# Kernel tuning notes

Hardware: AMD Instinct MI355X
Metric: run time of the kernel (lower is better)

## Reference

```python
import jax, jax.numpy as jnp
import numpy as np

BSZ, H, P, L = 8, 512, 128, 8192
DT_MIN, DT_MAX = 1e-3, 1e-1


def setup_inputs() -> dict:
    key = jax.random.key(0)
    ks = jax.random.split(key, 6)
    inp = {}
    inp["input_sequence"] = jax.random.normal(ks[0], (BSZ, 1, H, 1, L), jnp.float32)
    # HiPPO-like init: negative real parts, pi*k imaginary parts
    inp["Lambda_re"] = -jax.random.uniform(ks[1], (P,), jnp.float32, 0.1, 1.0)
    inp["Lambda_im"] = jnp.pi * jnp.arange(P, dtype=jnp.float32)
    # lecun_normal-ish: fan_in = H for B, fan_in = P for C (real+imag parts)
    inp["B"] = jax.random.normal(ks[2], (P, H, 2), jnp.float32) / np.float32(np.sqrt(2 * H))
    inp["C"] = jax.random.normal(ks[3], (H, P, 2), jnp.float32) / np.float32(np.sqrt(2 * P))
    inp["D"] = jax.random.normal(ks[4], (H,), jnp.float32)
    u01 = jax.random.uniform(ks[5], (P, 1), jnp.float32)
    inp["log_step"] = u01 * np.float32(np.log(DT_MAX) - np.log(DT_MIN)) + np.float32(np.log(DT_MIN))
    return inp


def _binary_operator(q_i, q_j):
    A_i, b_i = q_i
    A_j, b_j = q_j
    return (A_j * A_i, A_j * b_i + b_j)


def reference(input_sequence, Lambda_re, Lambda_im, B, C, D, log_step):
    # (bsz, 1, H, 1, L) -> (bsz, L, H)
    u = input_sequence[:, 0, :, 0].transpose(0, 2, 1)

    Lambda = Lambda_re + 1j * Lambda_im                      # (P,)
    B_tilde = B[..., 0] + 1j * B[..., 1]                     # (P, H)
    C_tilde = C[..., 0] + 1j * C[..., 1]                     # (H, P)
    step = jnp.exp(log_step[:, 0])                           # (P,)

    # zero-order hold discretization
    Lambda_bar = jnp.exp(Lambda * step)                      # (P,)
    B_bar = ((Lambda_bar - 1.0) / Lambda)[:, None] * B_tilde # (P, H)

    Bu = jnp.einsum('blh,ph->blp', u, B_bar)                 # (bsz, L, P) complex
    Lambda_elems = jnp.broadcast_to(Lambda_bar, Bu.shape)
    _, xs = jax.lax.associative_scan(_binary_operator, (Lambda_elems, Bu), axis=1)

    # conj_sym=True -> factor of 2 on the real part of emissions
    ys = 2.0 * jnp.einsum('blp,hp->blh', xs, C_tilde).real + D * u
    ys = jax.nn.gelu(ys, approximate=False)

    # back to (bsz, 1, H, 1, L)
    return ys.transpose(0, 2, 1)[:, None, :, None, :]
```

## Files before the change

### kernel.cpp

```cpp
#include <hip/hip_runtime.h>
#include <hip/hip_bf16.h>
#include <cmath>

namespace {
constexpr int Pn = 128;
constexpr int Hn = 512;
constexpr int Ln = 8192;
constexpr int BS = 8;
constexpr size_t OFF_BMAT = 2048;
constexpr size_t OFF_CMAT = 264192;
constexpr size_t OFF_PPOW = 526336;
constexpr size_t OFF_END  = 591872;
constexpr size_t OFF_CAR  = 1640448;
constexpr size_t HEADB    = 2689024;
constexpr size_t SZ_BU = (size_t)256 * Ln * 2;
}

typedef __attribute__((ext_vector_type(4))) float f32x4;
typedef __attribute__((ext_vector_type(8))) short bf16x8;

static __device__ inline short f2bf(float x) {
  __hip_bfloat16 h = __float2bfloat16(x);
  return *(short*)&h;
}
static __device__ inline float bf2f(short s) {
  unsigned u = ((unsigned)(unsigned short)s) << 16;
  return __uint_as_float(u);
}

static __device__ inline void async_copy16(const void* g, void* l) {
  __builtin_amdgcn_global_load_lds(
      (const __attribute__((address_space(1))) unsigned int*)g,
      (__attribute__((address_space(3))) unsigned int*)l, 16, 0, 0);
}

__global__ void precompute_kernel(const float* __restrict__ Lre,
                                  const float* __restrict__ Lim,
                                  const float* __restrict__ Bin,
                                  const float* __restrict__ Cin,
                                  const float* __restrict__ lstep,
                                  float* __restrict__ Lam,
                                  __hip_bfloat16* __restrict__ Bmat,
                                  __hip_bfloat16* __restrict__ Cmat,
                                  float* __restrict__ Ppow) {
  int tid = blockIdx.x * blockDim.x + threadIdx.x;
  if (tid < 2 * Pn * Hn) {
    int r = tid >> 9;
    int h = tid & (Hn - 1);
    int p = r & (Pn - 1);
    float st = expf(lstep[p]);
    float lr = Lre[p], li = Lim[p];
    float er = expf(lr * st);
    float cr = er * cosf(li * st);
    float ci = er * sinf(li * st);
    float nr = cr - 1.0f, ni = ci;
    float inv = 1.0f / (lr * lr + li * li);
    float wr = (nr * lr + ni * li) * inv;
    float wi = (ni * lr - nr * li) * inv;
    float btr = Bin[(p * Hn + h) * 2 + 0];
    float bti = Bin[(p * Hn + h) * 2 + 1];
    float val = (r < Pn) ? (wr * btr - wi * bti) : (wr * bti + wi * btr);
    Bmat[tid] = __float2bfloat16(val);
  } else if (tid < 4 * Pn * Hn) {
    int j = tid - 2 * Pn * Hn;
    int h = j >> 8;
    int c = j & 255;
    int p = c & (Pn - 1);
    float v = (c < Pn) ? 2.0f * Cin[(h * Pn + p) * 2 + 0]
                       : -2.0f * Cin[(h * Pn + p) * 2 + 1];
    Cmat[j] = __float2bfloat16(v);
  } else if (tid < 4 * Pn * Hn + 512) {
    int j = tid - 4 * Pn * Hn;
    int p = j & 127;
    int sel = j >> 7;
    float st = expf(lstep[p]);
    float lr = Lre[p], li = Lim[p];
    float sc = (sel < 2) ? st : 64.0f * st;
    float er = expf(lr * sc);
    Lam[(sel >> 1) * 256 + (sel & 1) * 128 + p] =
        (sel & 1) ? er * sinf(li * sc) : er * cosf(li * sc);
  } else if (tid < 4 * Pn * Hn + 512 + 64 * 256) {
    int j = tid - 4 * Pn * Hn - 512;
    int jr = j >> 8;
    int k = j & 255;
    int p = k & 127;
    float st = expf(lstep[p]);
    float lr = Lre[p], li = Lim[p];
    float tt = st * (float)(jr + 1);
    float er = expf(lr * tt);
    Ppow[j] = (k < 128) ? er * cosf(li * tt) : er * sinf(li * tt);
  }
}

__global__ __launch_bounds__(256) void gemm1_kernel(
    const __hip_bfloat16* __restrict__ Amat,
    const float* __restrict__ U,
    short* __restrict__ Bu,
    float* __restrict__ End,
    const float* __restrict__ Lam,
    int b0) {
  __shared__ __align__(16) char shm[33280];
  short* As = (short*)shm;
  short* Bsb = (short*)(shm + 16384);
  float (*Sl)[260] = (float(*)[260])shm;
  const int t = threadIdx.x;
  const int lane = t & 63, w = t >> 6;
  const int n0 = blockIdx.x * 64;
  const int bz = blockIdx.z;
  const float* Ub = U + (size_t)(b0 + bz) * Hn * Ln;

  const int srow = lane >> 2, scol = (lane & 3) * 16;
  const int bn = t & 63, bkg = t >> 6;
  const int lr = lane & 15, lk = (lane >> 4) * 8;

  f32x4 acc[4][4] = {};
  for (int k0 = 0; k0 < Hn; k0 += 32) {
#pragma unroll
    for (int I2 = 0; I2 < 4; I2++) {
      int I = 4 * w + I2;
      async_copy16((const char*)(Amat + (size_t)(16 * I + srow) * Hn + k0) + scol,
                   (char*)As + I * 1024);
    }
    {
      float v[8];
#pragma unroll
      for (int j = 0; j < 8; j++)
        v[j] = Ub[(size_t)(k0 + bkg * 8 + j) * Ln + n0 + bn];
      bf16x8 pk;
#pragma unroll
      for (int j = 0; j < 8; j++) pk[j] = f2bf(v[j]);
      *(bf16x8*)&Bsb[bn * 40 + bkg * 8] = pk;
    }
    __syncthreads();
    bf16x8 af[4], bfr[4];
#pragma unroll
    for (int mt = 0; mt < 4; mt++)
      af[mt] = *(const bf16x8*)&As[(64 * w + 16 * mt + lr) * 32 + lk];
#pragma unroll
    for (int nt = 0; nt < 4; nt++)
      bfr[nt] = *(const bf16x8*)&Bsb[(16 * nt + lr) * 40 + lk];
#pragma unroll
    for (int mt = 0; mt < 4; mt++)
#pragma unroll
      for (int nt = 0; nt < 4; nt++)
        acc[mt][nt] = __builtin_amdgcn_mfma_f32_16x16x32_bf16(
            af[mt], bfr[nt], acc[mt][nt], 0, 0, 0);
    __syncthreads();
  }

  const int row4 = (lane >> 4) * 4, col = lane & 15;
  short* Bub = Bu + (size_t)bz * Ln * 256;
  float scr = 0.f, sci = 0.f;
  const float Ar = Lam[t & 127], Ai = Lam[128 + (t & 127)];
#pragma unroll
  for (int pass = 0; pass < 2; pass++) {
    __syncthreads();
#pragma unroll
    for (int mt = 0; mt < 4; mt++)
#pragma unroll
      for (int ntl = 0; ntl < 2; ntl++) {
        int nt = 2 * pass + ntl;
        *(f32x4*)&Sl[16 * ntl + col][64 * w + 16 * mt + row4] = acc[mt][nt];
      }
    __syncthreads();
    if (t < 128) {
      const int p = t;
#pragma unroll
      for (int j = 0; j < 32; j++) {
        float br = Sl[j][p], bi = Sl[j][128 + p];
        float nr = fmaf(Ar, scr, fmaf(-Ai, sci, br));
        float ni = fmaf(Ar, sci, fmaf(Ai, scr, bi));
        scr = nr; sci = ni;
        Sl[j][p] = nr; Sl[j][128 + p] = ni;
      }
    }
    __syncthreads();
    {
      const int row = t >> 3, seg = t & 7;
      short* dst = Bub + (size_t)(n0 + 32 * pass + row) * 256 + seg * 32;
      const float* src = &Sl[row][seg * 32];
#pragma unroll
      for (int q = 0; q < 4; q++) {
        bf16x8 pk;
#pragma unroll
        for (int j = 0; j < 8; j++) pk[j] = f2bf(src[8 * q + j]);
        *(bf16x8*)&dst[8 * q] = pk;
      }
    }
  }
  if (t < 128) {
    float* E = End + ((size_t)bz * 128 + blockIdx.x) * 256;
    E[t] = scr;
    E[128 + t] = sci;
  }
}

__global__ __launch_bounds__(128) void carry_kernel(const float* __restrict__ End,
                                                    float* __restrict__ Carry,
                                                    const float* __restrict__ Lam) {
  const int bz = blockIdx.x;
  const int p = threadIdx.x;
  const float a64r = Lam[256 + p], a64i = Lam[384 + p];
  const float* E = End + (size_t)bz * 128 * 256;
  float* C = Carry + (size_t)bz * 128 * 256;
  float xr = 0.f, xi = 0.f;
  float er0[4], ei0[4], er1[4], ei1[4];
#pragma unroll
  for (int q = 0; q < 4; q++) {
    er0[q] = E[(size_t)q * 256 + p];
    ei0[q] = E[(size_t)q * 256 + 128 + p];
  }
  for (int c0 = 0; c0 < 128; c0 += 8) {
#pragma unroll
    for (int q = 0; q < 4; q++) {
      er1[q] = E[(size_t)(c0 + 4 + q) * 256 + p];
      ei1[q] = E[(size_t)(c0 + 4 + q) * 256 + 128 + p];
    }
#pragma unroll
    for (int q = 0; q < 4; q++) {
      C[(size_t)(c0 + q) * 256 + p] = xr;
      C[(size_t)(c0 + q) * 256 + 128 + p] = xi;
      float nr = fmaf(a64r, xr, fmaf(-a64i, xi, er0[q]));
      float ni = fmaf(a64r, xi, fmaf(a64i, xr, ei0[q]));
      xr = nr; xi = ni;
    }
#pragma unroll
    for (int q = 0; q < 4; q++) {
      int cn = c0 + 8 + q;
      if (cn < 128) {
        er0[q] = E[(size_t)cn * 256 + p];
        ei0[q] = E[(size_t)cn * 256 + 128 + p];
      }
    }
#pragma unroll
    for (int q = 0; q < 4; q++) {
      C[(size_t)(c0 + 4 + q) * 256 + p] = xr;
      C[(size_t)(c0 + 4 + q) * 256 + 128 + p] = xi;
      float nr = fmaf(a64r, xr, fmaf(-a64i, xi, er1[q]));
      float ni = fmaf(a64r, xi, fmaf(a64i, xr, ei1[q]));
      xr = nr; xi = ni;
    }
  }
}

__global__ __launch_bounds__(256) void gemm2_kernel(
    const __hip_bfloat16* __restrict__ Cmat,
    const short* __restrict__ Xs,
    const float* __restrict__ Ppow,
    const float* __restrict__ Cy,
    const float* __restrict__ U,
    const float* __restrict__ Dv,
    float* __restrict__ Out, int b0) {
  __shared__ __align__(16) short As[128 * 32];
  __shared__ __align__(16) short Bs[128 * 40];
  const int t = threadIdx.x;
  const int lane = t & 63, w = t >> 6;
  const int wm = w >> 1, wn = w & 1;
  const int n0 = blockIdx.x * 128;
  const int m0 = blockIdx.y * 128;
  const int bz = blockIdx.z;
  const int b = b0 + bz;

  const int srow = lane >> 2, scol = (lane & 3) * 16;
  const int krow = t >> 2, kq = t & 3;
  const short* Xb = Xs + ((size_t)bz * Ln + n0) * 256;
  const float* Cyb = Cy + ((size_t)bz * 128 + (n0 >> 6)) * 256;

  f32x4 acc[4][4] = {};
  for (int k0 = 0; k0 < 256; k0 += 32) {
#pragma unroll
    for (int I2 = 0; I2 < 2; I2++) {
      int I = 2 * w + I2;
      async_copy16((const char*)(Cmat + (size_t)(m0 + 16 * I + srow) * 256 + k0) + scol,
                   (char*)As + I * 1024);
    }
    {
      const int kw = k0 + kq * 8;
      const bool isRe = kw < 128;
      const int p0 = kw & 127;
#pragma unroll
      for (int ro = 0; ro < 2; ro++) {
        const int row = ro * 64 + krow;
        const int j = row & 63;
        bf16x8 xl = *(const bf16x8*)&Xb[(size_t)row * 256 + kw];
        f32x4 Pre0 = *(const f32x4*)&Ppow[j * 256 + p0];
        f32x4 Pre1 = *(const f32x4*)&Ppow[j * 256 + p0 + 4];
        f32x4 Pim0 = *(const f32x4*)&Ppow[j * 256 + 128 + p0];
        f32x4 Pim1 = *(const f32x4*)&Ppow[j * 256 + 128 + p0 + 4];
        f32x4 cr0 = *(const f32x4*)&Cyb[ro * 256 + p0];
        f32x4 cr1 = *(const f32x4*)&Cyb[ro * 256 + p0 + 4];
        f32x4 ci0 = *(const f32x4*)&Cyb[ro * 256 + 128 + p0];
        f32x4 ci1 = *(const f32x4*)&Cyb[ro * 256 + 128 + p0 + 4];
        f32x4 ca0 = isRe ? cr0 : ci0;
        f32x4 ca1 = isRe ? cr1 : ci1;
        f32x4 cb0 = isRe ? -ci0 : cr0;
        f32x4 cb1 = isRe ? -ci1 : cr1;
        bf16x8 pk;
#pragma unroll
        for (int q = 0; q < 4; q++) {
          float v = fmaf(Pre0[q], ca0[q], fmaf(Pim0[q], cb0[q], bf2f(xl[q])));
          pk[q] = f2bf(v);
        }
#pragma unroll
        for (int q = 0; q < 4; q++) {
          float v = fmaf(Pre1[q], ca1[q], fmaf(Pim1[q], cb1[q], bf2f(xl[4 + q])));
          pk[4 + q] = f2bf(v);
        }
        *(bf16x8*)&Bs[row * 40 + kq * 8] = pk;
      }
    }
    __syncthreads();
    const int lr = lane & 15, lk = (lane >> 4) * 8;
    bf16x8 af[4], bfr[4];
#pragma unroll
    for (int mt = 0; mt < 4; mt++)
      af[mt] = *(const bf16x8*)&As[(64 * wm + 16 * mt + lr) * 32 + lk];
#pragma unroll
    for (int nt = 0; nt < 4; nt++)
      bfr[nt] = *(const bf16x8*)&Bs[(64 * wn + 16 * nt + lr) * 40 + lk];
#pragma unroll
    for (int mt = 0; mt < 4; mt++)
#pragma unroll
      for (int nt = 0; nt < 4; nt++)
        acc[mt][nt] = __builtin_amdgcn_mfma_f32_16x16x32_bf16(
            af[mt], bfr[nt], acc[mt][nt], 0, 0, 0);
    __syncthreads();
  }
  const int row4 = (lane >> 4) * 4, col = lane & 15;
#pragma unroll
  for (int mt = 0; mt < 4; mt++) {
#pragma unroll
    for (int r = 0; r < 4; r++) {
      int h = m0 + 64 * wm + 16 * mt + row4 + r;
      float dh = Dv[h];
      const float* Urow = U + ((size_t)b * Hn + h) * Ln;
      float* Orow = Out + ((size_t)b * Hn + h) * Ln;
#pragma unroll
      for (int nt = 0; nt < 4; nt++) {
        int n = n0 + 64 * wn + 16 * nt + col;
        float y = acc[mt][nt][r] + dh * Urow[n];
        float u2 = y * (0.7978845608f + 0.0356774081f * y * y);
        Orow[n] = y / (1.0f + __expf(-2.0f * u2));
      }
    }
  }
}

extern "C" void kernel_launch(void* const* d_in, const int* in_sizes, int n_in,
                              void* d_out, int out_size, void* d_ws, size_t ws_size,
                              hipStream_t stream) {
  const float* U   = (const float*)d_in[0];
  const float* Lre = (const float*)d_in[1];
  const float* Lim = (const float*)d_in[2];
  const float* Bin = (const float*)d_in[3];
  const float* Cin = (const float*)d_in[4];
  const float* Dv  = (const float*)d_in[5];
  const float* ls  = (const float*)d_in[6];
  float* out = (float*)d_out;

  char* wsb = (char*)d_ws;
  float* Lam = (float*)wsb;
  __hip_bfloat16* Bmat = (__hip_bfloat16*)(wsb + OFF_BMAT);
  __hip_bfloat16* Cmat = (__hip_bfloat16*)(wsb + OFF_CMAT);
  float* Ppow = (float*)(wsb + OFF_PPOW);
  float* End = (float*)(wsb + OFF_END);
  float* Cy  = (float*)(wsb + OFF_CAR);
  short* Bu  = (short*)(wsb + HEADB);

  int NB = 8;
  while (NB > 1 && ws_size < HEADB + (size_t)NB * SZ_BU)
    NB >>= 1;

  precompute_kernel<<<(4 * Pn * Hn + 512 + 64 * 256 + 255) / 256, 256, 0, stream>>>(
      Lre, Lim, Bin, Cin, ls, Lam, Bmat, Cmat, Ppow);

  for (int b0 = 0; b0 < BS; b0 += NB) {
    gemm1_kernel<<<dim3(Ln / 64, 1, NB), 256, 0, stream>>>(Bmat, U, Bu, End, Lam, b0);
    carry_kernel<<<dim3(NB), 128, 0, stream>>>(End, Cy, Lam);
    gemm2_kernel<<<dim3(Ln / 128, Hn / 128, NB), 256, 0, stream>>>(
        Cmat, Bu, Ppow, Cy, U, Dv, out, b0);
  }
}
```

Measured before the change: 352.4 us.

## Double-buffer gemm2 LDS tiles and stage carry vectors in shared memory

Restructures the gemm2 main loop into a double-buffered software pipeline. Global loads for the next K-step (Cmat async copy, Xs, Ppow) are issued before the MFMAs of the current step, and the B-tile correction is written into the alternate buffer afterward, cutting one barrier per iteration. The per-block carry vectors are loaded once into LDS instead of being re-read from global each step. Ppow is indexed by krow, which is the same as the old row&63 for both row offsets, so its loads are shared across the two rows. This doubles LDS use and raises register pressure.

```diff
diff --git a/kernel.cpp b/kernel.cpp
--- a/kernel.cpp
+++ b/kernel.cpp
@@ -251,8 +251,9 @@
     const float* __restrict__ U,
     const float* __restrict__ Dv,
     float* __restrict__ Out, int b0) {
-  __shared__ __align__(16) short As[128 * 32];
-  __shared__ __align__(16) short Bs[128 * 40];
+  __shared__ __align__(16) short As[2][128 * 32];
+  __shared__ __align__(16) short Bs[2][128 * 40];
+  __shared__ __align__(16) float CyS[512];
   const int t = threadIdx.x;
   const int lane = t & 63, w = t >> 6;
   const int wm = w >> 1, wn = w & 1;
@@ -264,68 +265,94 @@
   const int srow = lane >> 2, scol = (lane & 3) * 16;
   const int krow = t >> 2, kq = t & 3;
   const short* Xb = Xs + ((size_t)bz * Ln + n0) * 256;
-  const float* Cyb = Cy + ((size_t)bz * 128 + (n0 >> 6)) * 256;
-
-  f32x4 acc[4][4] = {};
-  for (int k0 = 0; k0 < 256; k0 += 32) {
+
+  bf16x8 xl[2];
+  f32x4 Pr[4];
+
+  auto STAGE_A = [&](int s, int buf) {
+    const int k0 = s * 32;
 #pragma unroll
     for (int I2 = 0; I2 < 2; I2++) {
       int I = 2 * w + I2;
       async_copy16((const char*)(Cmat + (size_t)(m0 + 16 * I + srow) * 256 + k0) + scol,
-                   (char*)As + I * 1024);
-    }
-    {
-      const int kw = k0 + kq * 8;
-      const bool isRe = kw < 128;
-      const int p0 = kw & 127;
-#pragma unroll
-      for (int ro = 0; ro < 2; ro++) {
-        const int row = ro * 64 + krow;
-        const int j = row & 63;
-        bf16x8 xl = *(const bf16x8*)&Xb[(size_t)row * 256 + kw];
-        f32x4 Pre0 = *(const f32x4*)&Ppow[j * 256 + p0];
-        f32x4 Pre1 = *(const f32x4*)&Ppow[j * 256 + p0 + 4];
-        f32x4 Pim0 = *(const f32x4*)&Ppow[j * 256 + 128 + p0];
-        f32x4 Pim1 = *(const f32x4*)&Ppow[j * 256 + 128 + p0 + 4];
-        f32x4 cr0 = *(const f32x4*)&Cyb[ro * 256 + p0];
-        f32x4 cr1 = *(const f32x4*)&Cyb[ro * 256 + p0 + 4];
-        f32x4 ci0 = *(const f32x4*)&Cyb[ro * 256 + 128 + p0];
-        f32x4 ci1 = *(const f32x4*)&Cyb[ro * 256 + 128 + p0 + 4];
-        f32x4 ca0 = isRe ? cr0 : ci0;
-        f32x4 ca1 = isRe ? cr1 : ci1;
-        f32x4 cb0 = isRe ? -ci0 : cr0;
-        f32x4 cb1 = isRe ? -ci1 : cr1;
-        bf16x8 pk;
-#pragma unroll
-        for (int q = 0; q < 4; q++) {
-          float v = fmaf(Pre0[q], ca0[q], fmaf(Pim0[q], cb0[q], bf2f(xl[q])));
-          pk[q] = f2bf(v);
-        }
-#pragma unroll
-        for (int q = 0; q < 4; q++) {
-          float v = fmaf(Pre1[q], ca1[q], fmaf(Pim1[q], cb1[q], bf2f(xl[4 + q])));
-          pk[4 + q] = f2bf(v);
-        }
-        *(bf16x8*)&Bs[row * 40 + kq * 8] = pk;
-      }
-    }
-    __syncthreads();
-    const int lr = lane & 15, lk = (lane >> 4) * 8;
+                   (char*)As[buf] + I * 1024);
+    }
+  };
+  auto STAGE_ISSUE = [&](int s) {
+    const int kwin = s * 32 + kq * 8;
+    const int p0 = kwin & 127;
+#pragma unroll
+    for (int ro = 0; ro < 2; ro++)
+      xl[ro] = *(const bf16x8*)&Xb[(size_t)(ro * 64 + krow) * 256 + kwin];
+    Pr[0] = *(const f32x4*)&Ppow[krow * 256 + p0];
+    Pr[1] = *(const f32x4*)&Ppow[krow * 256 + p0 + 4];
+    Pr[2] = *(const f32x4*)&Ppow[krow * 256 + 128 + p0];
+    Pr[3] = *(const f32x4*)&Ppow[krow * 256 + 128 + p0 + 4];
+  };
+  auto STAGE_WRITE = [&](int s, int buf) {
+    const int kwin = s * 32 + kq * 8;
+    const bool isRe = kwin < 128;
+    const int p0 = kwin & 127;
+    const int ha = isRe ? 0 : 128, hb = isRe ? 128 : 0;
+#pragma unroll
+    for (int ro = 0; ro < 2; ro++) {
+      f32x4 u0 = *(const f32x4*)&CyS[ro * 256 + ha + p0];
+      f32x4 u1 = *(const f32x4*)&CyS[ro * 256 + ha + p0 + 4];
+      f32x4 v0 = *(const f32x4*)&CyS[ro * 256 + hb + p0];
+      f32x4 v1 = *(const f32x4*)&CyS[ro * 256 + hb + p0 + 4];
+      if (isRe) { v0 = -v0; v1 = -v1; }
+      bf16x8 pk;
+#pragma unroll
+      for (int q = 0; q < 4; q++) {
+        float v = fmaf(Pr[0][q], u0[q], fmaf(Pr[2][q], v0[q], bf2f(xl[ro][q])));
+        pk[q] = f2bf(v);
+      }
+#pragma unroll
+      for (int q = 0; q < 4; q++) {
+        float v = fmaf(Pr[1][q], u1[q], fmaf(Pr[3][q], v1[q], bf2f(xl[ro][4 + q])));
+        pk[4 + q] = f2bf(v);
+      }
+      *(bf16x8*)&Bs[buf][(ro * 64 + krow) * 40 + kq * 8] = pk;
+    }
+  };
+
+  STAGE_A(0, 0);
+  STAGE_ISSUE(0);
+  {
+    const float* Cyb = Cy + ((size_t)bz * 128 + (n0 >> 6)) * 256;
+    CyS[t] = Cyb[t];
+    CyS[256 + t] = Cyb[256 + t];
+  }
+  __syncthreads();
+  STAGE_WRITE(0, 0);
+  __syncthreads();
+
+  const int lr = lane & 15, lk = (lane >> 4) * 8;
+  f32x4 acc[4][4] = {};
+#pragma unroll
+  for (int s = 0; s < 8; s++) {
+    const int cur = s & 1;
+    if (s < 7) {
+      STAGE_A(s + 1, cur ^ 1);
+      STAGE_ISSUE(s + 1);
+    }
     bf16x8 af[4], bfr[4];
 #pragma unroll
     for (int mt = 0; mt < 4; mt++)
-      af[mt] = *(const bf16x8*)&As[(64 * wm + 16 * mt + lr) * 32 + lk];
+      af[mt] = *(const bf16x8*)&As[cur][(64 * wm + 16 * mt + lr) * 32 + lk];
 #pragma unroll
     for (int nt = 0; nt < 4; nt++)
-      bfr[nt] = *(const bf16x8*)&Bs[(64 * wn + 16 * nt + lr) * 40 + lk];
+      bfr[nt] = *(const bf16x8*)&Bs[cur][(64 * wn + 16 * nt + lr) * 40 + lk];
 #pragma unroll
     for (int mt = 0; mt < 4; mt++)
 #pragma unroll
       for (int nt = 0; nt < 4; nt++)
         acc[mt][nt] = __builtin_amdgcn_mfma_f32_16x16x32_bf16(
             af[mt], bfr[nt], acc[mt][nt], 0, 0, 0);
-    __syncthreads();
-  }
+    if (s < 7) STAGE_WRITE(s + 1, cur ^ 1);
+    __syncthreads();
+  }
+
   const int row4 = (lane >> 4) * 4, col = lane & 15;
 #pragma unroll
   for (int mt = 0; mt < 4; mt++) {
```

Measured after the change: 335.3 us. 1.05x faster.
